# Kernel optimization log

Measured on AMD Instinct MI355X. Metric: run time of the kernel, lower is better.

## Reference

```python
import jax, jax.numpy as jnp
import numpy as np

GRID_SIZE = 5
SPLINE_ORDER = 3
GRID_RANGE = (-1.0, 1.0)
NUM_SPLINES = 4096
BATCH = 4096


def make_grid():
    h = (GRID_RANGE[1] - GRID_RANGE[0]) / GRID_SIZE
    return jnp.linspace(GRID_RANGE[0] - SPLINE_ORDER * h,
                        GRID_RANGE[1] + SPLINE_ORDER * h,
                        GRID_SIZE + 2 * SPLINE_ORDER + 1, dtype=jnp.float32)


def setup_inputs() -> dict:
    key = jax.random.key(0)
    k1, k2 = jax.random.split(key)
    x = jax.random.uniform(k1, (BATCH, NUM_SPLINES), dtype=jnp.float32,
                           minval=-1.0, maxval=1.0)
    coefficients = jax.random.normal(k2, (NUM_SPLINES, GRID_SIZE + SPLINE_ORDER),
                                     dtype=jnp.float32) * 0.1
    grid = make_grid()
    return {"x": x, "coefficients": coefficients, "grid": grid}


def reference(x, coefficients, grid):
    # x: (B, S) -> (B, S, 1) for broadcasting against grid intervals
    xe = x[..., None]
    # order-0 indicator bases: (B, S, G-1) with G = 12
    bases = ((xe >= grid[:-1]) & (xe < grid[1:])).astype(x.dtype)
    eps = 1e-8
    for k in range(1, SPLINE_ORDER + 1):  # Cox-de Boor recursion
        left = (xe - grid[:-(k + 1)]) / (grid[k:-1] - grid[:-(k + 1)] + eps)
        right = (grid[k + 1:] - xe) / (grid[k + 1:] - grid[1:-k] + eps)
        bases = left * bases[..., :-1] + right * bases[..., 1:]
    # weighted sum over the 8 basis functions per spline
    return jnp.einsum('bsk,sk->bs', bases, coefficients)
```

## Files before the change

kernel.cpp:

```cpp
#include <hip/hip_runtime.h>

#define S_DIM 4096
#define B_DIM 4096
#define TPB   256
#define COLS  4
#define ROWS  8

typedef float v4f __attribute__((ext_vector_type(4)));

__device__ __forceinline__ float bspline_eval(float xv, const float* c) {
    float u  = __builtin_fmaf(xv, 2.5f, 5.5f);
    float jf = floorf(u);
    jf = fminf(fmaxf(jf, 3.0f), 7.0f);
    float f  = u - jf;
    int   p  = (int)jf - 3;
    float f2 = f * f;
    float f3 = f2 * f;
    float om = 1.0f - f;
    float w0 = om * om * om * (1.0f / 6.0f);
    float w3 = f3 * (1.0f / 6.0f);
    float w1 = __builtin_fmaf(0.5f, f3, (2.0f / 3.0f) - f2);
    float w2 = 1.0f - w0 - w1 - w3;

    bool p4 = p >= 4;
    bool p2 = (p & 2) != 0;
    bool p1 = (p & 1) != 0;
    float t0 = p4 ? c[4] : c[0];
    float t1 = p4 ? c[5] : c[1];
    float t2 = p4 ? c[6] : c[2];
    float t3 = p4 ? c[7] : c[3];
    float t4 = c[4], t5 = c[5], t6 = c[6];
    float u0 = p2 ? t2 : t0;
    float u1 = p2 ? t3 : t1;
    float u2 = p2 ? t4 : t2;
    float u3 = p2 ? t5 : t3;
    float u4 = p2 ? t6 : t4;
    float g0 = p1 ? u1 : u0;
    float g1 = p1 ? u2 : u1;
    float g2 = p1 ? u3 : u2;
    float g3 = p1 ? u4 : u3;

    return __builtin_fmaf(w0, g0,
           __builtin_fmaf(w1, g1,
           __builtin_fmaf(w2, g2, w3 * g3)));
}

__global__ __launch_bounds__(TPB) void BSplineBasis_70446053589597_kernel(
    const float* __restrict__ x,
    const float* __restrict__ coef,
    float* __restrict__ out)
{
    const int s0 = (blockIdx.x * TPB + threadIdx.x) * COLS;
    const int b0 = blockIdx.y * ROWS;

    float c[COLS][8];
    #pragma unroll
    for (int j = 0; j < COLS; ++j) {
        const v4f lo = *reinterpret_cast<const v4f*>(coef + (size_t)(s0 + j) * 8);
        const v4f hi = *reinterpret_cast<const v4f*>(coef + (size_t)(s0 + j) * 8 + 4);
        c[j][0] = lo.x; c[j][1] = lo.y; c[j][2] = lo.z; c[j][3] = lo.w;
        c[j][4] = hi.x; c[j][5] = hi.y; c[j][6] = hi.z; c[j][7] = hi.w;
    }

    #pragma unroll 4
    for (int r = 0; r < ROWS; ++r) {
        const size_t off = (size_t)(b0 + r) * S_DIM + s0;
        const v4f xv = *reinterpret_cast<const v4f*>(x + off);
        v4f ov;
        ov.x = bspline_eval(xv.x, c[0]);
        ov.y = bspline_eval(xv.y, c[1]);
        ov.z = bspline_eval(xv.z, c[2]);
        ov.w = bspline_eval(xv.w, c[3]);
        __builtin_nontemporal_store(ov, reinterpret_cast<v4f*>(out + off));
    }
}

extern "C" void kernel_launch(void* const* d_in, const int* in_sizes, int n_in,
                              void* d_out, int out_size, void* d_ws, size_t ws_size,
                              hipStream_t stream) {
    const float* x    = (const float*)d_in[0];
    const float* coef = (const float*)d_in[1];
    float* out = (float*)d_out;

    dim3 block(TPB);
    dim3 grid(S_DIM / (TPB * COLS), B_DIM / ROWS);
    BSplineBasis_70446053589597_kernel<<<grid, block, 0, stream>>>(x, coef, out);
}
```

Before: 29.71 us.

## Precompute per-interval cubic polynomial coefficients in LDS and software-pipeline row loads

Each block converts its 256 splines' 8 coefficients into 5 per-interval cubic polynomials stored in shared memory. Per element evaluation then becomes a Horner cubic with one LDS vector load, replacing the weight computation and select tree. Blocks now cover 64 rows with a two-deep register prefetch of x. Nontemporal stores become regular stores. The risk is LDS bank conflicts from the data-dependent reads at stride 20 and fewer blocks in the grid.

```diff
diff --git a/kernel.cpp b/kernel.cpp
--- a/kernel.cpp
+++ b/kernel.cpp
@@ -3,75 +3,78 @@
 #define S_DIM 4096
 #define B_DIM 4096
 #define TPB   256
-#define COLS  4
-#define ROWS  8
+#define CBLK  256
+#define RBLK  64
+#define RPASS 4
+#define NPASS (RBLK / RPASS)
 
 typedef float v4f __attribute__((ext_vector_type(4)));
 
-__device__ __forceinline__ float bspline_eval(float xv, const float* c) {
-    float u  = __builtin_fmaf(xv, 2.5f, 5.5f);
-    float jf = floorf(u);
-    jf = fminf(fmaxf(jf, 3.0f), 7.0f);
-    float f  = u - jf;
-    int   p  = (int)jf - 3;
-    float f2 = f * f;
-    float f3 = f2 * f;
-    float om = 1.0f - f;
-    float w0 = om * om * om * (1.0f / 6.0f);
-    float w3 = f3 * (1.0f / 6.0f);
-    float w1 = __builtin_fmaf(0.5f, f3, (2.0f / 3.0f) - f2);
-    float w2 = 1.0f - w0 - w1 - w3;
-
-    bool p4 = p >= 4;
-    bool p2 = (p & 2) != 0;
-    bool p1 = (p & 1) != 0;
-    float t0 = p4 ? c[4] : c[0];
-    float t1 = p4 ? c[5] : c[1];
-    float t2 = p4 ? c[6] : c[2];
-    float t3 = p4 ? c[7] : c[3];
-    float t4 = c[4], t5 = c[5], t6 = c[6];
-    float u0 = p2 ? t2 : t0;
-    float u1 = p2 ? t3 : t1;
-    float u2 = p2 ? t4 : t2;
-    float u3 = p2 ? t5 : t3;
-    float u4 = p2 ? t6 : t4;
-    float g0 = p1 ? u1 : u0;
-    float g1 = p1 ? u2 : u1;
-    float g2 = p1 ? u3 : u2;
-    float g3 = p1 ? u4 : u3;
-
-    return __builtin_fmaf(w0, g0,
-           __builtin_fmaf(w1, g1,
-           __builtin_fmaf(w2, g2, w3 * g3)));
-}
 
 __global__ __launch_bounds__(TPB) void BSplineBasis_70446053589597_kernel(
     const float* __restrict__ x,
     const float* __restrict__ coef,
     float* __restrict__ out)
 {
-    const int s0 = (blockIdx.x * TPB + threadIdx.x) * COLS;
-    const int b0 = blockIdx.y * ROWS;
+    __shared__ float Ps[CBLK * 20];
 
-    float c[COLS][8];
+    const int tid = threadIdx.x;
+    const int cb  = blockIdx.x * CBLK;
+    const int rb  = blockIdx.y * RBLK;
+
+    {
+        const float* cp = coef + (size_t)(cb + tid) * 8;
+        const v4f lo = *reinterpret_cast<const v4f*>(cp);
+        const v4f hi = *reinterpret_cast<const v4f*>(cp + 4);
+        const float c8[8] = {lo.x, lo.y, lo.z, lo.w, hi.x, hi.y, hi.z, hi.w};
+        float* Pw = Ps + tid * 20;
+        #pragma unroll
+        for (int p = 0; p < 5; ++p) {
+            const float g0 = c8[p], g1 = c8[p + 1], g2 = c8[p + 2], g3 = c8[p + 3];
+            const float s02 = g0 + g2;
+            v4f e;
+            e.x = __builtin_fmaf(g1 - g2, 0.5f, (g3 - g0) * (1.0f / 6.0f));
+            e.y = __builtin_fmaf(s02, 0.5f, -g1);
+            e.z = (g2 - g0) * 0.5f;
+            e.w = __builtin_fmaf(4.0f, g1, s02) * (1.0f / 6.0f);
+            *reinterpret_cast<v4f*>(Pw + p * 4) = e;
+        }
+    }
+    __syncthreads();
+
+    const int cg = (tid & 63) * 4;
+    const int r0 = (tid >> 6);
+
+    const float* P0 = Ps + cg * 20;
+
+    auto evalp = [&](float xv, int j) -> float {
+        float u  = __builtin_fmaf(xv, 2.5f, 5.5f);
+        float jf = floorf(u);
+        jf = fminf(fmaxf(jf, 3.0f), 7.0f);
+        float f  = u - jf;
+        int   p  = (int)jf - 3;
+        const v4f e = *reinterpret_cast<const v4f*>(P0 + j * 20 + p * 4);
+        return __builtin_fmaf(__builtin_fmaf(__builtin_fmaf(e.x, f, e.y), f, e.z), f, e.w);
+    };
+
+    const size_t base = (size_t)(rb + r0) * S_DIM + cb + cg;
+
+    v4f xa = *reinterpret_cast<const v4f*>(x + base);
+    v4f xb = *reinterpret_cast<const v4f*>(x + base + (size_t)RPASS * S_DIM);
+
     #pragma unroll
-    for (int j = 0; j < COLS; ++j) {
-        const v4f lo = *reinterpret_cast<const v4f*>(coef + (size_t)(s0 + j) * 8);
-        const v4f hi = *reinterpret_cast<const v4f*>(coef + (size_t)(s0 + j) * 8 + 4);
-        c[j][0] = lo.x; c[j][1] = lo.y; c[j][2] = lo.z; c[j][3] = lo.w;
-        c[j][4] = hi.x; c[j][5] = hi.y; c[j][6] = hi.z; c[j][7] = hi.w;
-    }
-
-    #pragma unroll 4
-    for (int r = 0; r < ROWS; ++r) {
-        const size_t off = (size_t)(b0 + r) * S_DIM + s0;
-        const v4f xv = *reinterpret_cast<const v4f*>(x + off);
+    for (int i = 0; i < NPASS; ++i) {
+        v4f xn;
+        if (i + 2 < NPASS)
+            xn = *reinterpret_cast<const v4f*>(x + base + (size_t)(i + 2) * RPASS * S_DIM);
         v4f ov;
-        ov.x = bspline_eval(xv.x, c[0]);
-        ov.y = bspline_eval(xv.y, c[1]);
-        ov.z = bspline_eval(xv.z, c[2]);
-        ov.w = bspline_eval(xv.w, c[3]);
-        __builtin_nontemporal_store(ov, reinterpret_cast<v4f*>(out + off));
+        ov.x = evalp(xa.x, 0);
+        ov.y = evalp(xa.y, 1);
+        ov.z = evalp(xa.z, 2);
+        ov.w = evalp(xa.w, 3);
+        *reinterpret_cast<v4f*>(out + base + (size_t)i * RPASS * S_DIM) = ov;
+        xa = xb;
+        xb = xn;
     }
 }
 
@@ -83,6 +86,6 @@
     float* out = (float*)d_out;
 
     dim3 block(TPB);
-    dim3 grid(S_DIM / (TPB * COLS), B_DIM / ROWS);
+    dim3 grid(S_DIM / CBLK, B_DIM / RBLK);
     BSplineBasis_70446053589597_kernel<<<grid, block, 0, stream>>>(x, coef, out);
 }
```

New measurement: 30.44 us. 1.02x slower.
